# Kernel tuning notes

Hardware: AMD Instinct MI355X
Metric: run time of the kernel (lower is better)

## Reference

```python
import jax, jax.numpy as jnp
import numpy as np

ALPHA = 0.05
MAX_ITER = 200
TOL = 0.01
N = 64
M = 1
BATCH = 262144


def setup_inputs() -> dict:
    key = jax.random.key(0)
    pred_cost = jax.random.normal(key, (BATCH, N), dtype=jnp.float32)
    # constraint data (fixed buffers, match init_kwargs)
    A = np.ones((M, N), dtype=np.float32)
    b = np.full((M,), 32.0, dtype=np.float32)
    lb = np.zeros((N,), dtype=np.float32)
    ub = np.ones((N,), dtype=np.float32)
    # SVD-based pseudoinverse factors for equality projection
    U, s, VT = np.linalg.svd(A, full_matrices=False)
    s_inv = np.where(s >= 1e-6, 1.0 / s, 0.0).astype(np.float32)
    return {
        "pred_cost": pred_cost,
        "A": jnp.asarray(A),
        "b": jnp.asarray(b),
        "lb": jnp.asarray(lb),
        "ub": jnp.asarray(ub),
        "V": jnp.asarray(VT.T.astype(np.float32)),   # (n, m)
        "UT": jnp.asarray(U.T.astype(np.float32)),   # (m, m)
        "s_inv": jnp.asarray(s_inv),                 # (m,)
    }


def _project_box(z, lb, ub):
    return jnp.clip(z, lb, ub)


def _project_equality(w, A, b, V, UT, s_inv):
    # w: (B, n). residual r = A w^T - b, correction = V diag(s_inv) U^T r
    r = w @ A.T - b                      # (B, m)
    corr = ((r @ UT.T) * s_inv) @ V.T    # (B, n)
    return w - corr


def _dys_step(z, cost, A, b, lb, ub, V, UT, s_inv):
    x = _project_box(z, lb, ub)
    grad = cost + ALPHA * x              # grad of regularized objective
    y = _project_equality(2.0 * x - z - ALPHA * grad, A, b, V, UT, s_inv)
    return z - x + y


def _run_to_convergence(cost, A, b, lb, ub, V, UT, s_inv):
    lb_safe = jnp.where(jnp.isfinite(lb), lb, 0.0)
    ub_safe = jnp.where(jnp.isfinite(ub), ub, 1.0)
    z0 = jax.random.uniform(jax.random.key(1), cost.shape, dtype=cost.dtype)
    z0 = z0 * (ub_safe - lb_safe) + lb_safe

    def cond(state):
        i, z, diff = state
        return jnp.logical_and(i < MAX_ITER, diff > TOL)

    def body(state):
        i, z, _ = state
        z_new = _dys_step(z, cost, A, b, lb, ub, V, UT, s_inv)
        diff = jnp.max(jnp.linalg.norm(z_new - z, axis=1))
        return (i + 1, z_new, diff)

    _, z, _ = jax.lax.while_loop(cond, body, (jnp.int32(0), z0, jnp.float32(1e30)))
    return z


def reference(pred_cost, A, b, lb, ub, V, UT, s_inv):
    cost = pred_cost  # minimize=True
    # no-grad fixed-point iterations
    z = jax.lax.stop_gradient(
        _run_to_convergence(jax.lax.stop_gradient(cost), A, b, lb, ub, V, UT, s_inv)
    )
    # training branch: one differentiable DYS step (JFB), then box projection
    z = _dys_step(z, cost, A, b, lb, ub, V, UT, s_inv)
    sol = _project_box(z, lb, ub)
    return sol
```

## Files before the change

kernel.cpp:

```cpp
#include <hip/hip_runtime.h>
#include <cstdint>


#ifndef JAX_PARTITIONABLE
#define JAX_PARTITIONABLE 1
#endif

#define BATCHN 262144
#define MAXIT  200

#define RPW_A  16
#define PROBE_ROWS 8192
#define PROBE_WAVES (PROBE_ROWS / RPW_A)
#define NWAVES_A (BATCHN / RPW_A)

#define RPW_D  16
#define NWAVES_D (BATCHN / RPW_D)

#define K1 0.9975f
#define K2 1.9975f

typedef float v2f __attribute__((ext_vector_type(2)));

__device__ __forceinline__ void tf2x32(uint32_t x0, uint32_t x1,
                                       uint32_t& o0, uint32_t& o1) {
  const uint32_t k0 = 0u, k1 = 1u;
  const uint32_t k2 = 0x1BD11BDAu ^ k0 ^ k1;
  x0 += k0; x1 += k1;
#define TFR(r) { x0 += x1; x1 = (x1 << (r)) | (x1 >> (32 - (r))); x1 ^= x0; }
  TFR(13) TFR(15) TFR(26) TFR(6)   x0 += k1; x1 += k2 + 1u;
  TFR(17) TFR(29) TFR(16) TFR(24)  x0 += k2; x1 += k0 + 2u;
  TFR(13) TFR(15) TFR(26) TFR(6)   x0 += k0; x1 += k1 + 3u;
  TFR(17) TFR(29) TFR(16) TFR(24)  x0 += k1; x1 += k2 + 4u;
  TFR(13) TFR(15) TFR(26) TFR(6)   x0 += k2; x1 += k0 + 5u;
#undef TFR
  o0 = x0; o1 = x1;
}

__device__ __forceinline__ float z0_at(uint32_t f) {
  uint32_t b;
#if JAX_PARTITIONABLE
  uint32_t o0, o1;
  tf2x32(0u, f, o0, o1);
  b = o0 ^ o1;
#else
  const uint32_t H = 8388608u;
  uint32_t lo = (f < H) ? f : (f - H);
  uint32_t o0, o1;
  tf2x32(lo, lo + H, o0, o1);
  b = (f < H) ? o0 : o1;
#endif
  return __uint_as_float((b >> 9) | 0x3f800000u) - 1.0f;
}

template <int CTRL>
__device__ __forceinline__ float dpp_add(float v) {
  int s = __builtin_amdgcn_mov_dpp(__float_as_int(v), CTRL, 0xF, 0xF, true);
  return v + __int_as_float(s);
}

__device__ __forceinline__ float reduce4(float v) {
  v = dpp_add<0xB1>(v);
  v = dpp_add<0x4E>(v);
  return v;
}


__device__ __forceinline__ float chk_iter_A(float U[16], const float c[16],
                                            float& CC, float& R) {
  const float Ch = CC + 20.0f;
  float sp[4] = {0.0f, 0.0f, 0.0f, 0.0f};
  float q1a = 0.0f, q1b = 0.0f, q2a = 0.0f, q2b = 0.0f;
#pragma unroll
  for (int j = 0; j < 16; ++j) {
    float m = __builtin_amdgcn_fmed3f(U[j], CC, Ch);
    sp[j & 3] += m;
    float un = __builtin_fmaf(K1, m, -c[j]);
    float d = un - U[j];
    if (j & 1) { q1b += d; q2b = __builtin_fmaf(d, d, q2b); }
    else       { q1a += d; q2a = __builtin_fmaf(d, d, q2a); }
    U[j] = un;
  }
  float s = (sp[0] + sp[1]) + (sp[2] + sp[3]);
  s = reduce4(s);
  float Sx = 0.05f * __builtin_fmaf(-64.0f, CC, s);
  float t  = __builtin_fmaf(K2, Sx, -R);
  float corr20 = __builtin_fmaf(t, 0.3125f, -10.0f);
  R = (R - Sx) + 32.0f;
  float CCn = __builtin_fmaf(K1, CC, corr20);
  float dCC = CCn - CC;
  CC = CCn;
  float q1 = reduce4(q1a + q1b);
  float q2 = reduce4(q2a + q2b);
  float a = __builtin_fmaf(64.0f, dCC, -2.0f * q1);
  return __builtin_fmaf(dCC, a, q2);
}

__device__ __forceinline__ void load_c_A(const float* __restrict__ cost,
                                         int base, float c[16]) {
#pragma unroll
  for (int k = 0; k < 4; ++k) {
    const float4 cq = *(const float4*)(cost + base + 4 * k);
    c[4 * k + 0] = cq.x; c[4 * k + 1] = cq.y;
    c[4 * k + 2] = cq.z; c[4 * k + 3] = cq.w;
  }
}

__device__ __forceinline__ void pin16(float v[16]) {
#pragma unroll
  for (int j = 0; j < 16; ++j) asm("" : "+v"(v[j]));
}

__device__ __forceinline__ void init_state_A(const float* __restrict__ cost,
                                             int base, float c[16],
                                             float U[16], float& CC,
                                             float& R) {
  load_c_A(cost, base, c);
  float r = 0.0f;
#pragma unroll
  for (int j = 0; j < 16; ++j) {
    float z0 = z0_at((uint32_t)(base + j));
    U[j] = 20.0f * z0;
    r = __builtin_fmaf(0.05f, c[j], r + z0);
  }
  pin16(c);
  pin16(U);
  R = reduce4(r);
  CC = 0.0f;
}

__global__ __launch_bounds__(256, 4) void dys_probe(
    const float* __restrict__ cost, int* __restrict__ Tsample) {
  const int lane = threadIdx.x & 63;
  const int gw = blockIdx.x * 4 + (threadIdx.x >> 6);
  const int base = (gw * RPW_A + (lane >> 2)) * 64 + (lane & 3) * 16;

  float c[16], U[16], CC, R;
  init_state_A(cost, base, c, U, CC, R);

  int ib = MAXIT;
  for (int i = 1; i <= MAXIT; ++i) {
    float ds = chk_iter_A(U, c, CC, R);
    if (__all(ds <= 0.04f)) { ib = i; break; }
  }
  if (lane == 0) atomicMax(Tsample, ib);
}


#define P8(X) X(0) X(1) X(2) X(3) X(4) X(5) X(6) X(7)

#define PAIRS4(X) X(0,0,1) X(1,2,3) X(2,4,5) X(3,6,7)

#define DECL_STATE(p) v2f U##p, nc##p;

#define PIN(p) asm("" : "+v"(U##p), "+v"(nc##p));

#define LOADC(k, p0, p1) { \
  const float4 cq = *(const float4*)(cost + base + 4 * (k)); \
  nc##p0.x = -cq.x; nc##p0.y = -cq.y; nc##p1.x = -cq.z; nc##p1.y = -cq.w; }

#define INITU(p) { \
  const float za = z0_at((uint32_t)(base + 2 * (p))); \
  const float zb = z0_at((uint32_t)(base + 2 * (p) + 1)); \
  U##p.x = 20.0f * za; U##p.y = 20.0f * zb; \
  r0 = __builtin_fmaf(-0.05f, nc##p.x, r0 + za); \
  r1 = __builtin_fmaf(-0.05f, nc##p.y, r1 + zb); }

#define FSTEP(p) { v2f m2; \
  m2.x = __builtin_amdgcn_fmed3f(U##p.x, CC, Ch); \
  m2.y = __builtin_amdgcn_fmed3f(U##p.y, CC, Ch); \
  if ((p) & 1) spB += m2; else spA += m2; \
  U##p = __builtin_elementwise_fma(K1p, m2, nc##p); }

#define FAST_ITER() { \
  const float Ch = CC + 20.0f; \
  v2f spA = {0.0f, 0.0f}, spB = {0.0f, 0.0f}; \
  P8(FSTEP) \
  const v2f spc = spA + spB; \
  const float s_ = reduce4(spc.x + spc.y); \
  const float Sx = 0.05f * __builtin_fmaf(-64.0f, CC, s_); \
  const float t_ = __builtin_fmaf(K2, Sx, -R); \
  const float corr20 = __builtin_fmaf(t_, 0.3125f, -10.0f); \
  R = (R - Sx) + 32.0f; \
  CC = __builtin_fmaf(K1, CC, corr20); }

#define CSTEP(p) { v2f m2; \
  m2.x = __builtin_amdgcn_fmed3f(U##p.x, CC, Ch); \
  m2.y = __builtin_amdgcn_fmed3f(U##p.y, CC, Ch); \
  if ((p) & 1) spB += m2; else spA += m2; \
  const v2f un2 = __builtin_elementwise_fma(K1p, m2, nc##p); \
  const v2f d2 = un2 - U##p; \
  q1v += d2; \
  q2v = __builtin_elementwise_fma(d2, d2, q2v); \
  U##p = un2; }

#define CHK_ITER(DS) { \
  const float Ch = CC + 20.0f; \
  v2f spA = {0.0f, 0.0f}, spB = {0.0f, 0.0f}; \
  v2f q1v = {0.0f, 0.0f}, q2v = {0.0f, 0.0f}; \
  P8(CSTEP) \
  const v2f spc = spA + spB; \
  const float s_ = reduce4(spc.x + spc.y); \
  const float Sx = 0.05f * __builtin_fmaf(-64.0f, CC, s_); \
  const float t_ = __builtin_fmaf(K2, Sx, -R); \
  const float corr20 = __builtin_fmaf(t_, 0.3125f, -10.0f); \
  R = (R - Sx) + 32.0f; \
  const float CCn = __builtin_fmaf(K1, CC, corr20); \
  const float dCC = CCn - CC; CC = CCn; \
  const float q1 = reduce4(q1v.x + q1v.y); \
  const float q2 = reduce4(q2v.x + q2v.y); \
  const float a_ = __builtin_fmaf(64.0f, dCC, -2.0f * q1); \
  DS = __builtin_fmaf(dCC, a_, q2); }

#define STZ(k, p0, p1) { float4 zq; \
  zq.x = __builtin_fmaf(0.05f, U##p0.x, -CC05); \
  zq.y = __builtin_fmaf(0.05f, U##p0.y, -CC05); \
  zq.z = __builtin_fmaf(0.05f, U##p1.x, -CC05); \
  zq.w = __builtin_fmaf(0.05f, U##p1.y, -CC05); \
  *(float4*)(zst + base + 4 * (k)) = zq; }

#define LOADZ(k, p0, p1) { \
  const float4 zq = *(const float4*)(zst + base + 4 * (k)); \
  U##p0.x = 20.0f * zq.x; U##p0.y = 20.0f * zq.y; \
  U##p1.x = 20.0f * zq.z; U##p1.y = 20.0f * zq.w; \
  r0 += zq.x + zq.y; r1 += zq.z + zq.w; }

#define RC(p) { r0 = __builtin_fmaf(-0.05f, nc##p.x, r0); \
  r1 = __builtin_fmaf(-0.05f, nc##p.y, r1); }

#define STOUT(k, p0, p1) { float4 o; \
  o.x = __builtin_amdgcn_fmed3f( \
      __builtin_fmaf(0.05f, U##p0.x, -CC05), 0.0f, 1.0f); \
  o.y = __builtin_amdgcn_fmed3f( \
      __builtin_fmaf(0.05f, U##p0.y, -CC05), 0.0f, 1.0f); \
  o.z = __builtin_amdgcn_fmed3f( \
      __builtin_fmaf(0.05f, U##p1.x, -CC05), 0.0f, 1.0f); \
  o.w = __builtin_amdgcn_fmed3f( \
      __builtin_fmaf(0.05f, U##p1.y, -CC05), 0.0f, 1.0f); \
  *(float4*)(out + base + 4 * (k)) = o; }

__global__ __attribute__((amdgpu_flat_work_group_size(256, 256),
                          amdgpu_waves_per_eu(4, 8)))
void dys_pass1(
    const float* __restrict__ cost, const int* __restrict__ Tsample,
    int* __restrict__ Tglob, int* __restrict__ TrArr,
    float* __restrict__ zst) {
  const int lane = threadIdx.x & 63;
  const int gw = blockIdx.x * 4 + (threadIdx.x >> 6);
  const int base = (gw * RPW_D + (lane >> 2)) * 64 + (lane & 3) * 16;

  const v2f K1p = {K1, K1};
  P8(DECL_STATE)
  PAIRS4(LOADC)
  float r0 = 0.0f, r1 = 0.0f;
  P8(INITU)
  P8(PIN)
  float R = reduce4(r0 + r1);
  float CC = 0.0f;

  const int Ts = *Tsample;
  const int Pn = (Ts > 2) ? (Ts - 2) : 0;

  for (int i = 0; i < Pn; ++i) FAST_ITER();

  int ib = MAXIT;
  for (int i = Pn + 1; i <= MAXIT; ++i) {
    float ds;
    CHK_ITER(ds)
    if (__all(ds <= 0.04f)) { ib = i; break; }
  }

  const float CC05 = 0.05f * CC;
  PAIRS4(STZ)
  if (lane == 0) {
    TrArr[gw] = ib;
    atomicMax(Tglob, ib);
  }
}

__global__ __attribute__((amdgpu_flat_work_group_size(256, 256),
                          amdgpu_waves_per_eu(4, 8)))
void dys_pass2(
    const float* __restrict__ cost, const int* __restrict__ Tglob,
    const int* __restrict__ TrArr, const float* __restrict__ zst,
    float* __restrict__ out) {
  const int lane = threadIdx.x & 63;
  const int gw = blockIdx.x * 4 + (threadIdx.x >> 6);
  const int base = (gw * RPW_D + (lane >> 2)) * 64 + (lane & 3) * 16;

  const v2f K1p = {K1, K1};
  P8(DECL_STATE)
  PAIRS4(LOADC)
  float r0 = 0.0f, r1 = 0.0f;
  PAIRS4(LOADZ)
  P8(RC)
  P8(PIN)
  float R = reduce4(r0 + r1);
  float CC = 0.0f;

  const int T = *Tglob;
  const int ib = TrArr[gw];

  for (int i = ib; i <= T; ++i) FAST_ITER();

  const float CC05 = 0.05f * CC;
  PAIRS4(STOUT)
}

extern "C" void kernel_launch(void* const* d_in, const int* in_sizes, int n_in,
                              void* d_out, int out_size, void* d_ws,
                              size_t ws_size, hipStream_t stream) {
  const float* cost = (const float*)d_in[0];
  float* out = (float*)d_out;

  int* Tglob   = (int*)d_ws;
  int* Tsample = (int*)d_ws + 1;
  const size_t TR_OFF = 1024;
  const size_t Z_OFF  = TR_OFF + (size_t)NWAVES_A * sizeof(int);
  int*   TrArr = (int*)((char*)d_ws + TR_OFF);
  float* zst   = (float*)((char*)d_ws + Z_OFF);

  hipMemsetAsync(d_ws, 0, 8, stream);

  dim3 block(256);
  dys_probe<<<dim3(PROBE_WAVES / 4), block, 0, stream>>>(cost, Tsample);
  dys_pass1<<<dim3(NWAVES_D / 4), block, 0, stream>>>(cost, Tsample, Tglob,
                                                      TrArr, zst);
  dys_pass2<<<dim3(NWAVES_D / 4), block, 0, stream>>>(cost, Tglob, TrArr, zst,
                                                      out);
}
```

Baseline: 385.9 us.

## Spread probe rows over 16 lanes with packed math and block-level max

The probe kernel now gives each row 16 lanes holding 4 elements each, instead of 4 lanes holding 16. This cuts per-lane serial work in the iteration loop, and the loop uses packed v2f FMAs. The sum of differences q1 is derived algebraically from running U-sums instead of being accumulated per element. The per-wave atomicMax is replaced by a shared-memory block max followed by one atomic per block. The cost is more launched waves (2048 vs 512) and longer DPP reduction chains per iteration.

```diff
diff --git a/kernel.cpp b/kernel.cpp
--- a/kernel.cpp
+++ b/kernel.cpp
@@ -9,10 +9,11 @@
 #define BATCHN 262144
 #define MAXIT  200
 
-#define RPW_A  16
 #define PROBE_ROWS 8192
-#define PROBE_WAVES (PROBE_ROWS / RPW_A)
-#define NWAVES_A (BATCHN / RPW_A)
+#define RPW_P  4
+#define PROBE_WAVES_P (PROBE_ROWS / RPW_P)
+
+#define NWAVES_A 16384
 
 #define RPW_D  16
 #define NWAVES_D (BATCHN / RPW_D)
@@ -65,85 +66,104 @@
   return v;
 }
 
-
-__device__ __forceinline__ float chk_iter_A(float U[16], const float c[16],
-                                            float& CC, float& R) {
-  const float Ch = CC + 20.0f;
-  float sp[4] = {0.0f, 0.0f, 0.0f, 0.0f};
-  float q1a = 0.0f, q1b = 0.0f, q2a = 0.0f, q2b = 0.0f;
-#pragma unroll
-  for (int j = 0; j < 16; ++j) {
-    float m = __builtin_amdgcn_fmed3f(U[j], CC, Ch);
-    sp[j & 3] += m;
-    float un = __builtin_fmaf(K1, m, -c[j]);
-    float d = un - U[j];
-    if (j & 1) { q1b += d; q2b = __builtin_fmaf(d, d, q2b); }
-    else       { q1a += d; q2a = __builtin_fmaf(d, d, q2a); }
-    U[j] = un;
-  }
-  float s = (sp[0] + sp[1]) + (sp[2] + sp[3]);
-  s = reduce4(s);
-  float Sx = 0.05f * __builtin_fmaf(-64.0f, CC, s);
-  float t  = __builtin_fmaf(K2, Sx, -R);
-  float corr20 = __builtin_fmaf(t, 0.3125f, -10.0f);
-  R = (R - Sx) + 32.0f;
-  float CCn = __builtin_fmaf(K1, CC, corr20);
-  float dCC = CCn - CC;
-  CC = CCn;
-  float q1 = reduce4(q1a + q1b);
-  float q2 = reduce4(q2a + q2b);
-  float a = __builtin_fmaf(64.0f, dCC, -2.0f * q1);
-  return __builtin_fmaf(dCC, a, q2);
-}
-
-__device__ __forceinline__ void load_c_A(const float* __restrict__ cost,
-                                         int base, float c[16]) {
-#pragma unroll
-  for (int k = 0; k < 4; ++k) {
-    const float4 cq = *(const float4*)(cost + base + 4 * k);
-    c[4 * k + 0] = cq.x; c[4 * k + 1] = cq.y;
-    c[4 * k + 2] = cq.z; c[4 * k + 3] = cq.w;
-  }
-}
-
-__device__ __forceinline__ void pin16(float v[16]) {
-#pragma unroll
-  for (int j = 0; j < 16; ++j) asm("" : "+v"(v[j]));
-}
-
-__device__ __forceinline__ void init_state_A(const float* __restrict__ cost,
-                                             int base, float c[16],
-                                             float U[16], float& CC,
-                                             float& R) {
-  load_c_A(cost, base, c);
-  float r = 0.0f;
-#pragma unroll
-  for (int j = 0; j < 16; ++j) {
-    float z0 = z0_at((uint32_t)(base + j));
-    U[j] = 20.0f * z0;
-    r = __builtin_fmaf(0.05f, c[j], r + z0);
-  }
-  pin16(c);
-  pin16(U);
-  R = reduce4(r);
-  CC = 0.0f;
+template <int CTRL>
+__device__ __forceinline__ v2f dpp_addv(v2f v) {
+  int sx = __builtin_amdgcn_mov_dpp(__float_as_int(v.x), CTRL, 0xF, 0xF, true);
+  int sy = __builtin_amdgcn_mov_dpp(__float_as_int(v.y), CTRL, 0xF, 0xF, true);
+  v2f s;
+  s.x = __int_as_float(sx);
+  s.y = __int_as_float(sy);
+  return v + s;
+}
+
+__device__ __forceinline__ v2f reduce16v(v2f v) {
+  v = dpp_addv<0xB1>(v);
+  v = dpp_addv<0x4E>(v);
+  v = dpp_addv<0x124>(v);
+  v = dpp_addv<0x128>(v);
+  return v;
 }
 
 __global__ __launch_bounds__(256, 4) void dys_probe(
     const float* __restrict__ cost, int* __restrict__ Tsample) {
   const int lane = threadIdx.x & 63;
-  const int gw = blockIdx.x * 4 + (threadIdx.x >> 6);
-  const int base = (gw * RPW_A + (lane >> 2)) * 64 + (lane & 3) * 16;
-
-  float c[16], U[16], CC, R;
-  init_state_A(cost, base, c, U, CC, R);
+  const int wid  = threadIdx.x >> 6;
+  const int gw = blockIdx.x * 4 + wid;
+  const int base = (gw * RPW_P + (lane >> 4)) * 64 + (lane & 15) * 4;
+
+  const v2f K1p = {K1, K1};
+  const float4 cq = *(const float4*)(cost + base);
+  v2f nc0, nc1;
+  nc0.x = -cq.x; nc0.y = -cq.y; nc1.x = -cq.z; nc1.y = -cq.w;
+
+  const float z0 = z0_at((uint32_t)(base + 0));
+  const float z1 = z0_at((uint32_t)(base + 1));
+  const float z2 = z0_at((uint32_t)(base + 2));
+  const float z3 = z0_at((uint32_t)(base + 3));
+  v2f U0, U1;
+  U0.x = 20.0f * z0; U0.y = 20.0f * z1;
+  U1.x = 20.0f * z2; U1.y = 20.0f * z3;
+
+  v2f zc;
+  zc.x = (z0 + z1) + (z2 + z3);
+  zc.y = (cq.x + cq.y) + (cq.z + cq.w);
+  zc = reduce16v(zc);
+  float R   = __builtin_fmaf(0.05f, zc.y, zc.x);
+  const float Snc = -zc.y;
+  float SU  = 20.0f * zc.x;
+  float CC = 0.0f;
 
   int ib = MAXIT;
   for (int i = 1; i <= MAXIT; ++i) {
-    float ds = chk_iter_A(U, c, CC, R);
+    const float Ch = CC + 20.0f;
+    v2f sp, q2v = {0.0f, 0.0f};
+    v2f m2, un2, d2;
+    m2.x = __builtin_amdgcn_fmed3f(U0.x, CC, Ch);
+    m2.y = __builtin_amdgcn_fmed3f(U0.y, CC, Ch);
+    sp = m2;
+    un2 = __builtin_elementwise_fma(K1p, m2, nc0);
+    d2 = un2 - U0;
+    q2v = __builtin_elementwise_fma(d2, d2, q2v);
+    U0 = un2;
+    m2.x = __builtin_amdgcn_fmed3f(U1.x, CC, Ch);
+    m2.y = __builtin_amdgcn_fmed3f(U1.y, CC, Ch);
+    sp += m2;
+    un2 = __builtin_elementwise_fma(K1p, m2, nc1);
+    d2 = un2 - U1;
+    q2v = __builtin_elementwise_fma(d2, d2, q2v);
+    U1 = un2;
+
+    v2f red;
+    red.x = sp.x + sp.y;
+    red.y = q2v.x + q2v.y;
+    red = reduce16v(red);
+    const float s_ = red.x;
+    const float q2 = red.y;
+
+    const float SUn = __builtin_fmaf(K1, s_, Snc);
+    const float q1 = SUn - SU;
+    SU = SUn;
+
+    const float Sx = 0.05f * __builtin_fmaf(-64.0f, CC, s_);
+    const float t_ = __builtin_fmaf(K2, Sx, -R);
+    const float corr20 = __builtin_fmaf(t_, 0.3125f, -10.0f);
+    R = (R - Sx) + 32.0f;
+    const float CCn = __builtin_fmaf(K1, CC, corr20);
+    const float dCC = CCn - CC;
+    CC = CCn;
+    const float a_ = __builtin_fmaf(64.0f, dCC, -2.0f * q1);
+    const float ds = __builtin_fmaf(dCC, a_, q2);
     if (__all(ds <= 0.04f)) { ib = i; break; }
   }
-  if (lane == 0) atomicMax(Tsample, ib);
+
+  __shared__ int ibs[4];
+  if (lane == 0) ibs[wid] = ib;
+  __syncthreads();
+  if (threadIdx.x == 0) {
+    const int m01 = ibs[0] > ibs[1] ? ibs[0] : ibs[1];
+    const int m23 = ibs[2] > ibs[3] ? ibs[2] : ibs[3];
+    atomicMax(Tsample, m01 > m23 ? m01 : m23);
+  }
 }
 
 
@@ -323,7 +343,7 @@
   hipMemsetAsync(d_ws, 0, 8, stream);
 
   dim3 block(256);
-  dys_probe<<<dim3(PROBE_WAVES / 4), block, 0, stream>>>(cost, Tsample);
+  dys_probe<<<dim3(PROBE_WAVES_P / 4), block, 0, stream>>>(cost, Tsample);
   dys_pass1<<<dim3(NWAVES_D / 4), block, 0, stream>>>(cost, Tsample, Tglob,
                                                       TrArr, zst);
   dys_pass2<<<dim3(NWAVES_D / 4), block, 0, stream>>>(cost, Tglob, TrArr, zst,
```

After: 368.9 us, median of 2. 4.4% less time.
